# Optimization experiments

Hardware: AMD Instinct MI355X
Metric: run time of the kernel (lower is better)

Reference implementation:

```python
import math
import jax, jax.numpy as jnp
import numpy as np

EPS = 1.0
TAU = 0.95
KAPPA = (1.0 - TAU) / 2.0
XI = (1.0 - TAU) / (1.0 + TAU)
RHO = EPS * TAU / (1.0 - TAU)
NUM_ITER = 10
B, H, WD, CC = 4, 128, 512, 64


def setup_inputs() -> dict:
    key = jax.random.key(0)
    C = jax.random.normal(key, (B, H, WD, CC), dtype=jnp.float32)
    return {"C": C}


def _lse(x, axis):
    return jax.nn.logsumexp(x, axis=axis)


def _softmax_lse(Cm, f, g, axis):
    # S = (C - f[...,None] - g[...,None,:]) / eps ; return eps*logsumexp(-S, axis)
    S = (Cm - f[..., None] - g[..., None, :]) / EPS
    return EPS * _lse(-S, axis)


def _lse_kernel(Cm, f, g, axis):
    w_res = _softmax_lse(Cm, f, g, axis)
    w_sgn = f if axis == -1 else g
    return w_res - jnp.where(jnp.isfinite(w_sgn), w_sgn, jnp.zeros_like(w_sgn))


def _sinkhorn_update(Cm, f, g, axis, log_marginal):
    app = _lse_kernel(Cm, f, g, axis)
    return EPS * log_marginal - jnp.where(jnp.isfinite(app), app, jnp.zeros_like(app))


def _smin(h, log_marginal):
    # smin(h, c) = -rho * logsumexp(-h/rho + log c, axis=-1)
    return -RHO * _lse(-h / RHO + log_marginal, -1)


def reference(C):
    b, h, wd, cc = C.shape
    log_a = jnp.full((wd,), -math.log(wd), dtype=C.dtype)  # row marginal (uniform)
    log_b = jnp.full((cc,), -math.log(cc), dtype=C.dtype)  # col marginal (uniform)

    # init potentials
    f = -EPS * _lse(-C / EPS + log_b, -1)       # (B,H,W)
    g = jnp.zeros((b, h, cc), dtype=C.dtype)    # (B,H,C)

    for _ in range(NUM_ITER):
        old_f = f
        new_g = TAU * _sinkhorn_update(C, old_f, g, -2, log_b)
        new_g = new_g - KAPPA * _smin(old_f, log_a)[..., None]
        new_g = new_g + XI * _smin(new_g, log_b)[..., None]
        new_f = TAU * _sinkhorn_update(C, f, new_g, -1, log_a)
        new_f = new_f - KAPPA * _smin(new_g, log_b)[..., None]
        new_f = new_f + XI * _smin(new_f, log_a)[..., None]
        f, g = new_f, new_g

    S = (C - f[..., None] - g[..., None, :]) / EPS
    return jnp.exp(-S)
```

## Files before the change

kernel.cpp:

```cpp
#include <hip/hip_runtime.h>


#define WD_ 512
#define CC_ 64
#define NITER_ 10
#define LP 68

__global__ __launch_bounds__(512, 1)
void uot_sinkhorn_kernel(const float* __restrict__ C, float* __restrict__ out) {
    constexpr float TAU   = 0.95f;
    constexpr float KAPPA = 0.025f;
    constexpr float XI    = 0.05f / 1.95f;
    constexpr float RHO   = 19.0f;
    constexpr float INV_RHO = 1.0f / 19.0f;
    const float log_a = -6.2383246250395075f;
    const float log_b = -4.1588830833596715f;

    __shared__ __align__(16) float Es[WD_ * LP];
    __shared__ __align__(16) float us[WD_];
    __shared__ __align__(16) float vs[CC_];
    __shared__ __align__(16) float ps[8 * CC_];
    __shared__ __align__(16) float red[8];

    const int tid  = threadIdx.x;
    const int lane = tid & 63;
    const int wv   = tid >> 6;

    const size_t base = (size_t)blockIdx.x * (WD_ * CC_);
    const float4* Cg4   = reinterpret_cast<const float4*>(C + base);
    float4*       outg4 = reinterpret_cast<float4*>(out + base);

    #pragma unroll
    for (int i = 0; i < 16; ++i) {
        int fi = i * 512 + tid;
        float4 v = Cg4[fi];
        int w  = fi >> 4;
        int c0 = (fi & 15) << 2;
        float4 e;
        e.x = __expf(-v.x); e.y = __expf(-v.y);
        e.z = __expf(-v.z); e.w = __expf(-v.w);
        *reinterpret_cast<float4*>(&Es[w * LP + c0]) = e;
    }
    __syncthreads();

    float4 ER[16];
    #pragma unroll
    for (int k = 0; k < 16; ++k)
        ER[k] = *reinterpret_cast<const float4*>(&Es[tid * LP + 4 * k]);

    float sminF;
    {
        float s0 = 0.f, s1 = 0.f, s2 = 0.f, s3 = 0.f;
        #pragma unroll
        for (int k = 0; k < 16; ++k) {
            s0 += ER[k].x; s1 += ER[k].y; s2 += ER[k].z; s3 += ER[k].w;
        }
        float fv = -(log_b + __logf((s0 + s1) + (s2 + s3)));
        us[tid] = __expf(fv);

        float x = __expf(-fv * INV_RHO);
        #pragma unroll
        for (int off = 32; off > 0; off >>= 1) x += __shfl_xor(x, off, 64);
        if (lane == 0) red[wv] = x;
        __syncthreads();
        float R = ((red[0] + red[1]) + (red[2] + red[3]))
                + ((red[4] + red[5]) + (red[6] + red[7]));
        sminF = -RHO * (log_a + __logf(R));
    }
    __syncthreads();

    const int r  = lane >> 4;
    const int cg = lane & 15;
    const int w0 = wv * 64;

    for (int it = 0; it < NITER_; ++it) {
        {
            float4 acc; acc.x = 0.f; acc.y = 0.f; acc.z = 0.f; acc.w = 0.f;
            #pragma unroll
            for (int j = 0; j < 16; ++j) {
                int w = w0 + 4 * j + r;
                float uw = us[w];
                float4 e = *reinterpret_cast<const float4*>(&Es[w * LP + 4 * cg]);
                acc.x += uw * e.x; acc.y += uw * e.y;
                acc.z += uw * e.z; acc.w += uw * e.w;
            }
            acc.x += __shfl_xor(acc.x, 16, 64); acc.y += __shfl_xor(acc.y, 16, 64);
            acc.z += __shfl_xor(acc.z, 16, 64); acc.w += __shfl_xor(acc.w, 16, 64);
            acc.x += __shfl_xor(acc.x, 32, 64); acc.y += __shfl_xor(acc.y, 32, 64);
            acc.z += __shfl_xor(acc.z, 32, 64); acc.w += __shfl_xor(acc.w, 32, 64);
            if (lane < 16)
                *reinterpret_cast<float4*>(&ps[wv * 64 + 4 * cg]) = acc;
        }
        __syncthreads();

        if (wv == 0) {
            float S = 0.f;
            #pragma unroll
            for (int k = 0; k < 8; ++k) S += ps[k * 64 + lane];
            float appg = __logf(S);
            float ng2  = TAU * (log_b - appg) - KAPPA * sminF;
            float t = __expf(-ng2 * INV_RHO);
            #pragma unroll
            for (int off = 32; off > 0; off >>= 1) t += __shfl_xor(t, off, 64);
            float sminG2 = -RHO * (log_b + __logf(t));
            vs[lane] = __expf(ng2 + XI * sminG2);
            if (lane == 0) red[0] = (1.0f + XI) * sminG2;
        }
        __syncthreads();
        const float sminG = red[0];

        float s0 = 0.f, s1 = 0.f, s2 = 0.f, s3 = 0.f;
        #pragma unroll
        for (int k = 0; k < 16; ++k) {
            float4 v4 = *reinterpret_cast<const float4*>(&vs[4 * k]);
            s0 += v4.x * ER[k].x; s1 += v4.y * ER[k].y;
            s2 += v4.z * ER[k].z; s3 += v4.w * ER[k].w;
        }
        float appf = __logf((s0 + s1) + (s2 + s3));
        float nf2  = TAU * (log_a - appf) - KAPPA * sminG;

        float x = __expf(-nf2 * INV_RHO);
        #pragma unroll
        for (int off = 32; off > 0; off >>= 1) x += __shfl_xor(x, off, 64);
        if (lane == 0) red[wv] = x;
        __syncthreads();
        float R = ((red[0] + red[1]) + (red[2] + red[3]))
                + ((red[4] + red[5]) + (red[6] + red[7]));
        float sminF2 = -RHO * (log_a + __logf(R));
        us[tid] = __expf(nf2 + XI * sminF2);
        sminF = (1.0f + XI) * sminF2;
        __syncthreads();
    }

    #pragma unroll
    for (int i = 0; i < 16; ++i) {
        int fi = i * 512 + tid;
        int w  = fi >> 4;
        int c0 = (fi & 15) << 2;
        float uw = us[w];
        float4 vv = *reinterpret_cast<const float4*>(&vs[c0]);
        float4 e  = *reinterpret_cast<const float4*>(&Es[w * LP + c0]);
        float4 o;
        o.x = uw * vv.x * e.x; o.y = uw * vv.y * e.y;
        o.z = uw * vv.z * e.z; o.w = uw * vv.w * e.w;
        outg4[fi] = o;
    }
}

extern "C" void kernel_launch(void* const* d_in, const int* in_sizes, int n_in,
                              void* d_out, int out_size, void* d_ws, size_t ws_size,
                              hipStream_t stream) {
    const float* C = (const float*)d_in[0];
    float* out = (float*)d_out;
    uot_sinkhorn_kernel<<<dim3(512), dim3(512), 0, stream>>>(C, out);
}
```

Baseline: 153.4 us.

## Store exp(-C) as fp16 in LDS and cut per-iteration barriers to one

The cached exp(-C) matrix now lives in LDS as fp16 instead of fp32, which halves its footprint so more blocks can share a CU (launch bounds raised to 4). Each iteration now needs one barrier instead of three. The row-scale softmin shift is folded into the next iteration, every wave redundantly computes the column update into its own buffer, u values are broadcast with shuffles instead of LDS, and the reduction slots are double-buffered. The costs are fp16 rounding of exp(-C), which can underflow or lose precision for large costs, and redundant column math in every wave.

```diff
diff --git a/kernel.cpp b/kernel.cpp
--- a/kernel.cpp
+++ b/kernel.cpp
@@ -1,12 +1,13 @@
 #include <hip/hip_runtime.h>
+#include <hip/hip_fp16.h>
 
 
 #define WD_ 512
 #define CC_ 64
 #define NITER_ 10
-#define LP 68
+#define LPH 72
 
-__global__ __launch_bounds__(512, 1)
+__global__ __launch_bounds__(512, 4)
 void uot_sinkhorn_kernel(const float* __restrict__ C, float* __restrict__ out) {
     constexpr float TAU   = 0.95f;
     constexpr float KAPPA = 0.025f;
@@ -16,15 +17,17 @@
     const float log_a = -6.2383246250395075f;
     const float log_b = -4.1588830833596715f;
 
-    __shared__ __align__(16) float Es[WD_ * LP];
-    __shared__ __align__(16) float us[WD_];
-    __shared__ __align__(16) float vs[CC_];
-    __shared__ __align__(16) float ps[8 * CC_];
-    __shared__ __align__(16) float red[8];
+    __shared__ __align__(16) unsigned short Es[WD_ * LPH];
+    __shared__ __align__(16) float vsb[8 * CC_];
+    __shared__ __align__(16) float ps[2][WD_];
+    __shared__ __align__(16) float red[2][8];
 
     const int tid  = threadIdx.x;
     const int lane = tid & 63;
     const int wv   = tid >> 6;
+    const int r    = lane >> 4;
+    const int cg   = lane & 15;
+    const int w0   = wv * 64;
 
     const size_t base = (size_t)blockIdx.x * (WD_ * CC_);
     const float4* Cg4   = reinterpret_cast<const float4*>(C + base);
@@ -36,19 +39,25 @@
         float4 v = Cg4[fi];
         int w  = fi >> 4;
         int c0 = (fi & 15) << 2;
-        float4 e;
-        e.x = __expf(-v.x); e.y = __expf(-v.y);
-        e.z = __expf(-v.z); e.w = __expf(-v.w);
-        *reinterpret_cast<float4*>(&Es[w * LP + c0]) = e;
+        __half2 h0 = __floats2half2_rn(__expf(-v.x), __expf(-v.y));
+        __half2 h1 = __floats2half2_rn(__expf(-v.z), __expf(-v.w));
+        uint2 pk;
+        *reinterpret_cast<__half2*>(&pk.x) = h0;
+        *reinterpret_cast<__half2*>(&pk.y) = h1;
+        *reinterpret_cast<uint2*>(&Es[w * LPH + c0]) = pk;
     }
     __syncthreads();
 
     float4 ER[16];
     #pragma unroll
-    for (int k = 0; k < 16; ++k)
-        ER[k] = *reinterpret_cast<const float4*>(&Es[tid * LP + 4 * k]);
+    for (int k = 0; k < 16; ++k) {
+        uint2 raw = *reinterpret_cast<const uint2*>(&Es[tid * LPH + 4 * k]);
+        float2 a = __half22float2(*reinterpret_cast<__half2*>(&raw.x));
+        float2 b = __half22float2(*reinterpret_cast<__half2*>(&raw.y));
+        ER[k] = make_float4(a.x, a.y, b.x, b.y);
+    }
 
-    float sminF;
+    float u_own;
     {
         float s0 = 0.f, s1 = 0.f, s2 = 0.f, s3 = 0.f;
         #pragma unroll
@@ -56,93 +65,96 @@
             s0 += ER[k].x; s1 += ER[k].y; s2 += ER[k].z; s3 += ER[k].w;
         }
         float fv = -(log_b + __logf((s0 + s1) + (s2 + s3)));
-        us[tid] = __expf(fv);
-
+        u_own = __expf(fv);
         float x = __expf(-fv * INV_RHO);
         #pragma unroll
         for (int off = 32; off > 0; off >>= 1) x += __shfl_xor(x, off, 64);
-        if (lane == 0) red[wv] = x;
-        __syncthreads();
-        float R = ((red[0] + red[1]) + (red[2] + red[3]))
-                + ((red[4] + red[5]) + (red[6] + red[7]));
-        sminF = -RHO * (log_a + __logf(R));
+        if (lane == 0) red[0][wv] = x;
     }
-    __syncthreads();
 
-    const int r  = lane >> 4;
-    const int cg = lane & 15;
-    const int w0 = wv * 64;
+    float xi_eff = 0.0f;
 
+    #pragma unroll 2
     for (int it = 0; it < NITER_; ++it) {
-        {
-            float4 acc; acc.x = 0.f; acc.y = 0.f; acc.z = 0.f; acc.w = 0.f;
-            #pragma unroll
-            for (int j = 0; j < 16; ++j) {
-                int w = w0 + 4 * j + r;
-                float uw = us[w];
-                float4 e = *reinterpret_cast<const float4*>(&Es[w * LP + 4 * cg]);
-                acc.x += uw * e.x; acc.y += uw * e.y;
-                acc.z += uw * e.z; acc.w += uw * e.w;
-            }
-            acc.x += __shfl_xor(acc.x, 16, 64); acc.y += __shfl_xor(acc.y, 16, 64);
-            acc.z += __shfl_xor(acc.z, 16, 64); acc.w += __shfl_xor(acc.w, 16, 64);
-            acc.x += __shfl_xor(acc.x, 32, 64); acc.y += __shfl_xor(acc.y, 32, 64);
-            acc.z += __shfl_xor(acc.z, 32, 64); acc.w += __shfl_xor(acc.w, 32, 64);
-            if (lane < 16)
-                *reinterpret_cast<float4*>(&ps[wv * 64 + 4 * cg]) = acc;
+        const int p = it & 1;
+
+        float ax = 0.f, ay = 0.f, az = 0.f, aw = 0.f;
+        #pragma unroll
+        for (int j = 0; j < 16; ++j) {
+            int row = w0 + 4 * j + r;
+            float uw = __shfl(u_own, 4 * j + r, 64);
+            uint2 raw = *reinterpret_cast<const uint2*>(&Es[row * LPH + 4 * cg]);
+            float2 a = __half22float2(*reinterpret_cast<__half2*>(&raw.x));
+            float2 b = __half22float2(*reinterpret_cast<__half2*>(&raw.y));
+            ax = fmaf(uw, a.x, ax); ay = fmaf(uw, a.y, ay);
+            az = fmaf(uw, b.x, az); aw = fmaf(uw, b.y, aw);
         }
+        ax += __shfl_xor(ax, 16, 64); ay += __shfl_xor(ay, 16, 64);
+        az += __shfl_xor(az, 16, 64); aw += __shfl_xor(aw, 16, 64);
+        ax += __shfl_xor(ax, 32, 64); ay += __shfl_xor(ay, 32, 64);
+        az += __shfl_xor(az, 32, 64); aw += __shfl_xor(aw, 32, 64);
+        if (lane < 16)
+            *reinterpret_cast<float4*>(&ps[p][w0 + 4 * cg]) =
+                make_float4(ax, ay, az, aw);
+
         __syncthreads();
 
-        if (wv == 0) {
-            float S = 0.f;
-            #pragma unroll
-            for (int k = 0; k < 8; ++k) S += ps[k * 64 + lane];
-            float appg = __logf(S);
-            float ng2  = TAU * (log_b - appg) - KAPPA * sminF;
-            float t = __expf(-ng2 * INV_RHO);
-            #pragma unroll
-            for (int off = 32; off > 0; off >>= 1) t += __shfl_xor(t, off, 64);
-            float sminG2 = -RHO * (log_b + __logf(t));
-            vs[lane] = __expf(ng2 + XI * sminG2);
-            if (lane == 0) red[0] = (1.0f + XI) * sminG2;
-        }
-        __syncthreads();
-        const float sminG = red[0];
+        float R = ((red[p][0] + red[p][1]) + (red[p][2] + red[p][3]))
+                + ((red[p][4] + red[p][5]) + (red[p][6] + red[p][7]));
+        float sminF2 = -RHO * (log_a + __logf(R));
+        float shift  = xi_eff * sminF2;
+        float sminF  = shift + sminF2;
+        float S = 0.f;
+        #pragma unroll
+        for (int k = 0; k < 8; ++k) S += ps[p][k * 64 + lane];
+        float appg = __logf(S) + shift;
+        float ng2  = TAU * (log_b - appg) - KAPPA * sminF;
+        float t = __expf(-ng2 * INV_RHO);
+        #pragma unroll
+        for (int off = 32; off > 0; off >>= 1) t += __shfl_xor(t, off, 64);
+        float sminG2 = -RHO * (log_b + __logf(t));
+        vsb[w0 + lane] = __expf(ng2 + XI * sminG2);
+        float sminG = (1.0f + XI) * sminG2;
 
         float s0 = 0.f, s1 = 0.f, s2 = 0.f, s3 = 0.f;
         #pragma unroll
         for (int k = 0; k < 16; ++k) {
-            float4 v4 = *reinterpret_cast<const float4*>(&vs[4 * k]);
-            s0 += v4.x * ER[k].x; s1 += v4.y * ER[k].y;
-            s2 += v4.z * ER[k].z; s3 += v4.w * ER[k].w;
+            float4 v4 = *reinterpret_cast<const float4*>(&vsb[w0 + 4 * k]);
+            s0 = fmaf(v4.x, ER[k].x, s0); s1 = fmaf(v4.y, ER[k].y, s1);
+            s2 = fmaf(v4.z, ER[k].z, s2); s3 = fmaf(v4.w, ER[k].w, s3);
         }
         float appf = __logf((s0 + s1) + (s2 + s3));
         float nf2  = TAU * (log_a - appf) - KAPPA * sminG;
-
+        u_own = __expf(nf2);
         float x = __expf(-nf2 * INV_RHO);
         #pragma unroll
         for (int off = 32; off > 0; off >>= 1) x += __shfl_xor(x, off, 64);
-        if (lane == 0) red[wv] = x;
-        __syncthreads();
-        float R = ((red[0] + red[1]) + (red[2] + red[3]))
-                + ((red[4] + red[5]) + (red[6] + red[7]));
+        if (lane == 0) red[p ^ 1][wv] = x;
+        xi_eff = XI;
+    }
+
+    __syncthreads();
+    {
+        float R = ((red[0][0] + red[0][1]) + (red[0][2] + red[0][3]))
+                + ((red[0][4] + red[0][5]) + (red[0][6] + red[0][7]));
         float sminF2 = -RHO * (log_a + __logf(R));
-        us[tid] = __expf(nf2 + XI * sminF2);
-        sminF = (1.0f + XI) * sminF2;
-        __syncthreads();
+        ps[1][tid] = u_own * __expf(XI * sminF2);
     }
+    __syncthreads();
 
     #pragma unroll
     for (int i = 0; i < 16; ++i) {
         int fi = i * 512 + tid;
         int w  = fi >> 4;
         int c0 = (fi & 15) << 2;
-        float uw = us[w];
-        float4 vv = *reinterpret_cast<const float4*>(&vs[c0]);
-        float4 e  = *reinterpret_cast<const float4*>(&Es[w * LP + c0]);
+        float uw = ps[1][w];
+        float4 vv = *reinterpret_cast<const float4*>(&vsb[w0 + c0]);
+        uint2 raw = *reinterpret_cast<const uint2*>(&Es[w * LPH + c0]);
+        float2 a = __half22float2(*reinterpret_cast<__half2*>(&raw.x));
+        float2 b = __half22float2(*reinterpret_cast<__half2*>(&raw.y));
         float4 o;
-        o.x = uw * vv.x * e.x; o.y = uw * vv.y * e.y;
-        o.z = uw * vv.z * e.z; o.w = uw * vv.w * e.w;
+        o.x = uw * vv.x * a.x; o.y = uw * vv.y * a.y;
+        o.z = uw * vv.z * b.x; o.w = uw * vv.w * b.y;
         outg4[fi] = o;
     }
 }
```

Result: no change. 154.4 us (+0.7%).
